# Performance work log

Hardware: AMD Instinct MI355X
Metric: run time of the kernel (lower is better)

Reference implementation:

```python
import jax, jax.numpy as jnp
import numpy as np

D_MODEL = 1024
HIDDEN = 4096
N_EXPERTS = 8
LB_COEF = 0.01
B, N = 2, 2048


def setup_inputs() -> dict:
    key = jax.random.key(0)
    k_x, k_g, k_w1, k_w2 = jax.random.split(key, 4)
    s = 0.02
    return {
        "x": jax.random.normal(k_x, (B, N, D_MODEL), dtype=jnp.float32),
        "gate_w": jax.random.normal(k_g, (N_EXPERTS, D_MODEL), dtype=jnp.float32) * s,
        "w1": jax.random.normal(k_w1, (N_EXPERTS, HIDDEN, D_MODEL), dtype=jnp.float32) * s,  # torch Linear weight [out,in]
        "b1": jnp.zeros((N_EXPERTS, HIDDEN), dtype=jnp.float32),
        "w2": jax.random.normal(k_w2, (N_EXPERTS, D_MODEL, HIDDEN), dtype=jnp.float32) * s,
        "b2": jnp.zeros((N_EXPERTS, D_MODEL), dtype=jnp.float32),
    }


def reference(x, gate_w, w1, b1, w2, b2):
    # gate logits: Linear(d_model, E, bias=False)
    logits = jnp.einsum('bnd,ed->bne', x, gate_w)
    probs = jax.nn.softmax(logits, axis=-1)            # router_prob
    gate_scores = jnp.max(probs, axis=-1)              # top-1 prob [B,N]
    sel = jnp.argmax(probs, axis=-1)                   # selected expert [B,N]

    # load-balance aux loss
    onehot = jax.nn.one_hot(sel, N_EXPERTS, dtype=x.dtype)
    f = onehot.mean(axis=(0, 1))                       # fraction of tokens per expert
    P = probs.mean(axis=(0, 1))                        # mean router prob per expert
    aux_loss = LB_COEF * N_EXPERTS * jnp.sum(f * P)

    # dispatch: loop over fixed small expert count (structurally distinct weights)
    out = jnp.zeros_like(x)
    for e in range(N_EXPERTS):
        h = jax.nn.gelu(jnp.einsum('bnd,hd->bnh', x, w1[e]) + b1[e], approximate=False)
        y = jnp.einsum('bnh,dh->bnd', h, w2[e]) + b2[e]
        out = out + jnp.where((sel == e)[..., None], gate_scores[..., None] * y, jnp.zeros((), x.dtype))
    return out, aux_loss
```

## Files before the change

kernel.cpp:

```cpp
#include <hip/hip_runtime.h>
#include <math.h>

#define T_TOK 4096
#define DM 1024
#define HID 4096
#define NEXP 8

typedef unsigned short u16;
typedef __attribute__((ext_vector_type(8))) short short8;
typedef __attribute__((ext_vector_type(4))) float f32x4;

__device__ __forceinline__ u16 f2bf(float f){
  unsigned u = __float_as_uint(f);
  u += 0x7FFF + ((u >> 16) & 1);
  return (u16)(u >> 16);
}

#define GATE_OFF   0u
#define CNT_OFF    16384u
#define LIST_OFF   16512u
#define PROBS_OFF  147584u
#define XB_OFF     278656u
#define H_OFF      8667264u
#define PART_OFF   42221696u

__device__ __forceinline__ void glds16(const void* g, void* l){
  __builtin_amdgcn_global_load_lds((const __attribute__((address_space(1))) void*)g,
                                   (__attribute__((address_space(3))) void*)l, 16, 0, 0);
}

__global__ void zero_cnt_kernel(int* cnt){
  if (threadIdx.x < NEXP) cnt[threadIdx.x] = 0;
}

__global__ __launch_bounds__(256) void gate_kernel(
    const float* __restrict__ x, const float* __restrict__ gw,
    float* __restrict__ gateo, int* __restrict__ cnt, int* __restrict__ list,
    float* __restrict__ probs, u16* __restrict__ xb)
{
  int tid = threadIdx.x;
  int lane = tid & 63;
  int w = tid >> 6;
  int t = blockIdx.x * 4 + w;

  const float4* x4 = (const float4*)(x + (size_t)t * DM);
  const float4* g4 = (const float4*)gw;

  float acc[8] = {0,0,0,0,0,0,0,0};
  #pragma unroll
  for (int i = 0; i < 4; i++){
    int p = i * 64 + lane;
    float4 xv = x4[p];
    ushort4 pk;
    pk.x = f2bf(xv.x); pk.y = f2bf(xv.y); pk.z = f2bf(xv.z); pk.w = f2bf(xv.w);
    *(ushort4*)&xb[(size_t)t * DM + (size_t)p * 4] = pk;
    #pragma unroll
    for (int e = 0; e < NEXP; e++){
      float4 gv = g4[e * 256 + p];
      acc[e] += xv.x * gv.x + xv.y * gv.y + xv.z * gv.z + xv.w * gv.w;
    }
  }
  #pragma unroll
  for (int e = 0; e < NEXP; e++){
    #pragma unroll
    for (int off = 32; off; off >>= 1)
      acc[e] += __shfl_xor(acc[e], off);
  }
  if (lane == 0){
    float mx = acc[0];
    #pragma unroll
    for (int e = 1; e < NEXP; e++) mx = fmaxf(mx, acc[e]);
    float p[8]; float s = 0.f;
    #pragma unroll
    for (int e = 0; e < NEXP; e++){ p[e] = expf(acc[e] - mx); s += p[e]; }
    float inv = 1.f / s;
    int be = 0; float bp = p[0];
    #pragma unroll
    for (int e = 1; e < NEXP; e++){ if (p[e] > bp){ bp = p[e]; be = e; } }
    #pragma unroll
    for (int e = 0; e < NEXP; e++) probs[(size_t)t * 8 + e] = p[e] * inv;
    gateo[t] = bp * inv;
    int pos = atomicAdd(&cnt[be], 1);
    list[be * T_TOK + pos] = t;
  }
}

__global__ __launch_bounds__(256) void aux_kernel(
    const float* __restrict__ probs, const int* __restrict__ cnt,
    float* __restrict__ aux_out)
{
  __shared__ float sm[256 * 8];
  int tid = threadIdx.x;
  float s[8] = {0,0,0,0,0,0,0,0};
  for (int i = 0; i < 16; i++){
    int t = i * 256 + tid;
    #pragma unroll
    for (int e = 0; e < 8; e++) s[e] += probs[(size_t)t * 8 + e];
  }
  #pragma unroll
  for (int e = 0; e < 8; e++) sm[tid * 8 + e] = s[e];
  __syncthreads();
  for (int st = 128; st; st >>= 1){
    if (tid < st){
      #pragma unroll
      for (int e = 0; e < 8; e++) sm[tid * 8 + e] += sm[(tid + st) * 8 + e];
    }
    __syncthreads();
  }
  if (tid == 0){
    float a = 0.f;
    #pragma unroll
    for (int e = 0; e < 8; e++){
      float f = (float)cnt[e] / (float)T_TOK;
      float P = sm[e] / (float)T_TOK;
      a += f * P;
    }
    aux_out[0] = 0.01f * (float)NEXP * a;
  }
}

template<int ASTR, int BSTR, int NTOT, int KS, bool PHASE2>
__global__ __launch_bounds__(256, 3) void ffn_gemm(
    const u16*  __restrict__ Aall,
    const float* __restrict__ Bf,
    const float* __restrict__ bias,
    const int*  __restrict__ cnt,
    const int*  __restrict__ list,
    u16*  __restrict__ hOut,
    float* __restrict__ pOut)
{
  int bid = blockIdx.x;
  int x  = bid & 7;
  int r  = bid >> 3;
  int j  = r & 31;
  int Wq = r >> 5;
  int W  = Wq * 8 + x;
  int dm = j >> 3, dn = j & 7;

  int e = -1, g = 0, c = 0, Te = 0, accW = 0;
  #pragma unroll
  for (int i = 0; i < NEXP; i++){
    int ti = (cnt[i] + 127) >> 7;
    int wi = ((ti + 3) >> 2) * 4;
    if (e < 0 && W < accW + wi){
      int Wl = W - accW; e = i; g = Wl >> 2; c = Wl & 3; Te = ti;
    }
    accW += wi;
  }
  if (e < 0) return;
  int mt = g * 4 + dm;
  if (mt >= Te) return;
  int ne = cnt[e];
  int m0 = mt * 128;
  const int* lst = list + e * T_TOK;
  int nt = PHASE2 ? dn : (c * 8 + dn);
  int sk = PHASE2 ? c : 0;
  int n0 = nt * 128;
  int koff = sk * (KS * 64);

  __shared__ u16 As[8192];
  __shared__ u16 Bs[8192];

  int tid  = threadIdx.x;
  int lane = tid & 63;
  int w    = tid >> 6;
  int wm = w >> 1, wn = w & 1;
  int fr = lane & 15, fq = lane >> 4;

  const u16* aS[4]; int aDst[4];
  #pragma unroll
  for (int i = 0; i < 4; i++){
    int seg = w * 4 + i;
    int rr  = seg * 8 + (lane >> 3);
    int gg  = (lane & 7) ^ (rr & 7);
    int mrow = m0 + rr; if (mrow > ne - 1) mrow = ne - 1;
    aS[i] = Aall + (size_t)lst[mrow] * ASTR + koff + gg * 8;
    aDst[i] = seg * 512;
  }

  const float* bS[4]; int bDst[4];
  #pragma unroll
  for (int i = 0; i < 4; i++){
    int cc = i * 256 + tid;
    int rr = cc >> 3, sl = cc & 7;
    int gg = sl ^ (rr & 7);
    bS[i] = Bf + ((size_t)e * NTOT + n0 + rr) * BSTR + koff + gg * 8;
    bDst[i] = rr * 64 + sl * 8;
  }

  f32x4 acc[4][4];
  #pragma unroll
  for (int m = 0; m < 4; m++)
    #pragma unroll
    for (int n = 0; n < 4; n++)
      acc[m][n] = (f32x4){0.f, 0.f, 0.f, 0.f};

  float4 br0[4], br1[4];
  #pragma unroll
  for (int i = 0; i < 4; i++){
    const float4* s = (const float4*)bS[i];
    br0[i] = s[0]; br1[i] = s[1];
  }

  for (int ks = 0; ks < KS; ++ks){
    if (ks) __syncthreads();
    size_t ko = (size_t)ks * 64;
    #pragma unroll
    for (int i = 0; i < 4; i++) glds16(aS[i] + ko, &As[aDst[i]]);
    #pragma unroll
    for (int i = 0; i < 4; i++){
      uint4 pk;
      pk.x = (unsigned)f2bf(br0[i].x) | ((unsigned)f2bf(br0[i].y) << 16);
      pk.y = (unsigned)f2bf(br0[i].z) | ((unsigned)f2bf(br0[i].w) << 16);
      pk.z = (unsigned)f2bf(br1[i].x) | ((unsigned)f2bf(br1[i].y) << 16);
      pk.w = (unsigned)f2bf(br1[i].z) | ((unsigned)f2bf(br1[i].w) << 16);
      *(uint4*)&Bs[bDst[i]] = pk;
    }
    if (ks + 1 < KS){
      #pragma unroll
      for (int i = 0; i < 4; i++){
        const float4* s = (const float4*)(bS[i] + (ks + 1) * 64);
        br0[i] = s[0]; br1[i] = s[1];
      }
    }
    __syncthreads();
    #pragma unroll
    for (int kc = 0; kc < 2; kc++){
      short8 afr[4], bfr[4];
      #pragma unroll
      for (int m = 0; m < 4; m++){
        int row  = wm * 64 + m * 16 + fr;
        int slot = (kc * 4 + fq) ^ (row & 7);
        afr[m] = *(const short8*)&As[row * 64 + slot * 8];
      }
      #pragma unroll
      for (int n = 0; n < 4; n++){
        int row  = wn * 64 + n * 16 + fr;
        int slot = (kc * 4 + fq) ^ (row & 7);
        bfr[n] = *(const short8*)&Bs[row * 64 + slot * 8];
      }
      #pragma unroll
      for (int m = 0; m < 4; m++)
        #pragma unroll
        for (int n = 0; n < 4; n++)
          acc[m][n] = __builtin_amdgcn_mfma_f32_16x16x32_bf16(afr[m], bfr[n], acc[m][n], 0, 0, 0);
    }
  }

  #pragma unroll
  for (int n = 0; n < 4; n++){
    int col = n0 + wn * 64 + n * 16 + fr;
    float bv = bias[(size_t)e * NTOT + col];
    if (PHASE2 && sk != 0) bv = 0.f;
    #pragma unroll
    for (int m = 0; m < 4; m++){
      int rbase = m0 + wm * 64 + m * 16 + fq * 4;
      f32x4 v = acc[m][n];
      #pragma unroll
      for (int i = 0; i < 4; i++){
        int mrow = rbase + i;
        if (mrow < ne){
          int tok = lst[mrow];
          float val = v[i] + bv;
          if (PHASE2){
            pOut[((size_t)sk * T_TOK + tok) * DM + col] = val;
          } else {
            float gl = 0.5f * val * (1.0f + erff(val * 0.70710678118654752f));
            hOut[(size_t)tok * HID + col] = f2bf(gl);
          }
        }
      }
    }
  }
}

__global__ __launch_bounds__(256) void reduce_kernel(
    const float* __restrict__ part, const float* __restrict__ gate,
    float* __restrict__ out)
{
  size_t i = (size_t)blockIdx.x * 256 + threadIdx.x;
  constexpr size_t S = (size_t)T_TOK * DM / 4;
  const float4* p = (const float4*)part;
  float4 a = p[i], b = p[i + S], c = p[i + 2 * S], d = p[i + 3 * S];
  float g = gate[i >> 8];
  float4 o;
  o.x = (a.x + b.x + c.x + d.x) * g;
  o.y = (a.y + b.y + c.y + d.y) * g;
  o.z = (a.z + b.z + c.z + d.z) * g;
  o.w = (a.w + b.w + c.w + d.w) * g;
  ((float4*)out)[i] = o;
}

extern "C" void kernel_launch(void* const* d_in, const int* in_sizes, int n_in,
                              void* d_out, int out_size, void* d_ws, size_t ws_size,
                              hipStream_t stream) {
  const float* x   = (const float*)d_in[0];
  const float* gw  = (const float*)d_in[1];
  const float* w1  = (const float*)d_in[2];
  const float* b1  = (const float*)d_in[3];
  const float* w2  = (const float*)d_in[4];
  const float* b2  = (const float*)d_in[5];

  char* ws = (char*)d_ws;
  float* gateo = (float*)(ws + GATE_OFF);
  int*   cnt   = (int*)  (ws + CNT_OFF);
  int*   list  = (int*)  (ws + LIST_OFF);
  float* probs = (float*)(ws + PROBS_OFF);
  u16*   xb    = (u16*)  (ws + XB_OFF);
  u16*   h     = (u16*)  (ws + H_OFF);
  float* part  = (float*)(ws + PART_OFF);

  float* out = (float*)d_out;
  float* aux = out + (size_t)T_TOK * DM;

  hipLaunchKernelGGL(zero_cnt_kernel, dim3(1), dim3(64), 0, stream, cnt);
  hipLaunchKernelGGL(gate_kernel, dim3(T_TOK / 4), dim3(256), 0, stream,
                     x, gw, gateo, cnt, list, probs, xb);
  hipLaunchKernelGGL(aux_kernel, dim3(1), dim3(256), 0, stream, probs, cnt, aux);

  hipLaunchKernelGGL((ffn_gemm<DM, DM, HID, 16, false>),
                     dim3(2048), dim3(256), 0, stream,
                     xb, w1, b1, cnt, list, h, (float*)nullptr);
  hipLaunchKernelGGL((ffn_gemm<HID, HID, DM, 16, true>),
                     dim3(2048), dim3(256), 0, stream,
                     h, w2, b2, cnt, list, (u16*)nullptr, part);
  hipLaunchKernelGGL(reduce_kernel, dim3(T_TOK * DM / 4 / 256), dim3(256), 0, stream,
                     part, gateo, out);
}
```

Baseline: 311.9 us.

## Remap GEMM block indexing to compact per-expert M-tiles and shrink grid

```diff
diff --git a/kernel.cpp b/kernel.cpp
--- a/kernel.cpp
+++ b/kernel.cpp
@@ -5,6 +5,7 @@
 #define DM 1024
 #define HID 4096
 #define NEXP 8
+#define MAXT 39
 
 typedef unsigned short u16;
 typedef __attribute__((ext_vector_type(8))) short short8;
@@ -119,7 +120,7 @@
   }
 }
 
-template<int ASTR, int BSTR, int NTOT, int KS, bool PHASE2>
+template<int ASTR, int BSTR, int NTOT, int GW, int KS, bool PHASE2>
 __global__ __launch_bounds__(256, 3) void ffn_gemm(
     const u16*  __restrict__ Aall,
     const float* __restrict__ Bf,
@@ -130,31 +131,24 @@
     float* __restrict__ pOut)
 {
   int bid = blockIdx.x;
-  int x  = bid & 7;
-  int r  = bid >> 3;
-  int j  = r & 31;
-  int Wq = r >> 5;
-  int W  = Wq * 8 + x;
-  int dm = j >> 3, dn = j & 7;
-
-  int e = -1, g = 0, c = 0, Te = 0, accW = 0;
+  int x   = bid & 7;
+  int r1  = bid >> 3;
+  int t   = r1 >> 2;
+  int inner = r1 & 3;
+  int nt = (GW == 4) ? (x * 4 + inner) : x;
+  int sk = (GW == 4) ? 0 : inner;
+
+  int e = -1, mt = 0, accT = 0;
   #pragma unroll
   for (int i = 0; i < NEXP; i++){
-    int ti = (cnt[i] + 127) >> 7;
-    int wi = ((ti + 3) >> 2) * 4;
-    if (e < 0 && W < accW + wi){
-      int Wl = W - accW; e = i; g = Wl >> 2; c = Wl & 3; Te = ti;
-    }
-    accW += wi;
+    int nti = (cnt[i] + 127) >> 7;
+    if (e < 0 && t < accT + nti){ e = i; mt = t - accT; }
+    accT += nti;
   }
   if (e < 0) return;
-  int mt = g * 4 + dm;
-  if (mt >= Te) return;
   int ne = cnt[e];
   int m0 = mt * 128;
   const int* lst = list + e * T_TOK;
-  int nt = PHASE2 ? dn : (c * 8 + dn);
-  int sk = PHASE2 ? c : 0;
   int n0 = nt * 128;
   int koff = sk * (KS * 64);
 
@@ -318,11 +312,11 @@
                      x, gw, gateo, cnt, list, probs, xb);
   hipLaunchKernelGGL(aux_kernel, dim3(1), dim3(256), 0, stream, probs, cnt, aux);
 
-  hipLaunchKernelGGL((ffn_gemm<DM, DM, HID, 16, false>),
-                     dim3(2048), dim3(256), 0, stream,
+  hipLaunchKernelGGL((ffn_gemm<DM, DM, HID, 4, 16, false>),
+                     dim3(8 * MAXT * 4), dim3(256), 0, stream,
                      xb, w1, b1, cnt, list, h, (float*)nullptr);
-  hipLaunchKernelGGL((ffn_gemm<HID, HID, DM, 16, true>),
-                     dim3(2048), dim3(256), 0, stream,
+  hipLaunchKernelGGL((ffn_gemm<HID, HID, DM, 1, 16, true>),
+                     dim3(8 * MAXT * 4), dim3(256), 0, stream,
                      h, w2, b2, cnt, list, (u16*)nullptr, part);
   hipLaunchKernelGGL(reduce_kernel, dim3(T_TOK * DM / 4 / 256), dim3(256), 0, stream,
                      part, gateo, out);
```

Result: no change. 306.0 us (-1.9%).
